# Performance work log

Hardware: AMD Instinct MI355X
Metric: run time of the kernel (lower is better)

Reference implementation:

```python
import jax, jax.numpy as jnp
import numpy as np

N_NODES = 100000
N_EDGES = 640000
NODE_D = 128   # node_emb_dim == edge_type_emb_dim (required by reverse-net input dim)
MSG_D = 128


def setup_inputs() -> dict:
    key = jax.random.key(0)
    ks = jax.random.split(key, 10)
    cat_d = 3 * NODE_D  # 2*node_emb + edge_type_emb
    s_msg = 1.0 / np.sqrt(cat_d)
    s_upd = 1.0 / np.sqrt(MSG_D)
    return {
        "node_features": jax.random.normal(ks[0], (N_NODES, NODE_D), jnp.float32),
        "edge_features": jax.random.normal(ks[1], (N_EDGES, NODE_D), jnp.float32),
        "from_idx": jax.random.randint(ks[2], (N_EDGES,), 0, N_NODES, jnp.int32),
        "to_idx": jax.random.randint(ks[3], (N_EDGES,), 0, N_NODES, jnp.int32),
        # message net (Linear + ReLU)
        "W_msg": jax.random.uniform(ks[4], (cat_d, MSG_D), jnp.float32, -s_msg, s_msg),
        "b_msg": jnp.zeros((MSG_D,), jnp.float32),
        # reverse message net (separate params)
        "W_rev": jax.random.uniform(ks[5], (cat_d, MSG_D), jnp.float32, -s_msg, s_msg),
        "b_rev": jnp.zeros((MSG_D,), jnp.float32),
        # node-update MLP (Linear + ReLU), residual update
        "W_upd": jax.random.uniform(ks[6], (MSG_D, NODE_D), jnp.float32, -s_upd, s_upd),
        "b_upd": jnp.zeros((NODE_D,), jnp.float32),
    }


def reference(node_features, edge_features, from_idx, to_idx,
              W_msg, b_msg, W_rev, b_rev, W_upd, b_upd):
    # gather endpoints and concat with edge features: [n_edges, 3*node_d]
    edge_inputs = jnp.concatenate(
        [node_features[from_idx], node_features[to_idx], edge_features], axis=-1)
    # forward + reverse message nets (same inputs, different params), summed
    messages = (jax.nn.relu(edge_inputs @ W_msg + b_msg)
                + jax.nn.relu(edge_inputs @ W_rev + b_rev))
    # scatter-sum into destination nodes: [n_nodes, msg_d]
    aggregated = jax.ops.segment_sum(messages, to_idx, num_segments=N_NODES)
    # residual node update: node + MLP(agg)
    return node_features + jax.nn.relu(aggregated @ W_upd + b_upd)
```

## Files before the change

kernel.cpp:

```cpp
#include <hip/hip_runtime.h>
#include <hip/hip_bf16.h>

#define N_NODES 100000
#define N_EDGES 640000

typedef __bf16 bf16_t;
typedef __bf16 bf16x8 __attribute__((ext_vector_type(8)));
typedef float f32x4 __attribute__((ext_vector_type(4)));
typedef float f4 __attribute__((ext_vector_type(4)));
typedef unsigned int u32x4 __attribute__((ext_vector_type(4)));

__device__ __forceinline__ float bflo(unsigned int u) { return __uint_as_float(u << 16); }
__device__ __forceinline__ float bfhi(unsigned int u) { return __uint_as_float(u & 0xffff0000u); }
__device__ __forceinline__ unsigned int bfpack(float a, float b) {
    union { bf16_t h[2]; unsigned int u; } pk;
    pk.h[0] = (bf16_t)a; pk.h[1] = (bf16_t)b;
    return pk.u;
}

__global__ void hist_kernel(const int* __restrict__ to_idx, int* __restrict__ hist) {
    int e = blockIdx.x * 256 + threadIdx.x;
    if (e < N_EDGES) atomicAdd(&hist[to_idx[e]], 1);
}

#define SCAN_CH 1000

__global__ __launch_bounds__(1024)
void scan_reduce_kernel(const int* __restrict__ hist, int* __restrict__ bsum) {
    __shared__ int red[1024];
    int b = blockIdx.x, t = threadIdx.x;
    int v = (t < SCAN_CH) ? hist[b * SCAN_CH + t] : 0;
    red[t] = v;
    __syncthreads();
    for (int off = 512; off > 0; off >>= 1) {
        if (t < off) red[t] += red[t + off];
        __syncthreads();
    }
    if (t == 0) bsum[b] = red[0];
}

__global__ __launch_bounds__(128)
void scan_base_kernel(const int* __restrict__ bsum, int* __restrict__ bbase) {
    __shared__ int s[128];
    int t = threadIdx.x;
    int v = (t < 100) ? bsum[t] : 0;
    s[t] = v;
    __syncthreads();
    for (int off = 1; off < 128; off <<= 1) {
        int u = (t >= off) ? s[t - off] : 0;
        __syncthreads();
        s[t] += u;
        __syncthreads();
    }
    if (t < 100) bbase[t] = s[t] - v;
}

__global__ __launch_bounds__(1024)
void scan_final_kernel(const int* __restrict__ hist,
                       const int* __restrict__ bbase,
                       int* __restrict__ cursor,
                       int* __restrict__ row_start) {
    __shared__ int s[1024];
    int b = blockIdx.x, t = threadIdx.x;
    int v = (t < SCAN_CH) ? hist[b * SCAN_CH + t] : 0;
    s[t] = v;
    __syncthreads();
    for (int off = 1; off < 1024; off <<= 1) {
        int u = (t >= off) ? s[t - off] : 0;
        __syncthreads();
        s[t] += u;
        __syncthreads();
    }
    int excl = bbase[b] + s[t] - v;
    if (t < SCAN_CH) {
        cursor[b * SCAN_CH + t] = excl;
        row_start[b * SCAN_CH + t] = excl;
    }
    if (b == 99 && t == SCAN_CH - 1) row_start[N_NODES] = excl + v;
}

__global__ void inv_scatter_kernel(const int* __restrict__ to_idx,
                                   int* __restrict__ cursor,
                                   int* __restrict__ inv) {
    int e = blockIdx.x * 256 + threadIdx.x;
    if (e < N_EDGES) {
        int pos = atomicAdd(&cursor[to_idx[e]], 1);
        inv[e] = pos;
    }
}

__global__ void prep_w_new(const float* __restrict__ Wmsg,
                           const float* __restrict__ Wrev,
                           const float* __restrict__ Wupd,
                           bf16_t* __restrict__ Wt1,
                           bf16_t* __restrict__ WtE,
                           bf16_t* __restrict__ WtU) {
    int idx = blockIdx.x * 256 + threadIdx.x;
    if (idx < 512 * 128) {
        int p = idx >> 7, k = idx & 127;
        int blk = p >> 7, c = p & 127;
        float v;
        if (blk == 0)      v = Wmsg[k * 128 + c];
        else if (blk == 1) v = Wrev[k * 128 + c];
        else if (blk == 2) v = Wmsg[(128 + k) * 128 + c];
        else               v = Wrev[(128 + k) * 128 + c];
        Wt1[idx] = (bf16_t)v;
    }
    if (idx < 256 * 128) {
        int p = idx >> 7, k = idx & 127;
        float v = (p < 128) ? Wmsg[(256 + k) * 128 + p]
                            : Wrev[(256 + k) * 128 + (p - 128)];
        WtE[idx] = (bf16_t)v;
    }
    if (idx < 128 * 128) {
        int n = idx >> 7, p = idx & 127;
        int colp = 32 * (p >> 5) + ((p >> 1) & 15) + 16 * (p & 1);
        WtU[idx] = (bf16_t)Wupd[colp * 128 + n];
    }
}

__global__ __launch_bounds__(512, 4)
void proj_node_kernel(const float* __restrict__ nodef,
                      const bf16_t* __restrict__ Wt1,
                      unsigned int* __restrict__ A_u) {
    __shared__ char lds_raw[64 * 256];
    const int tid = threadIdx.x;
    const int nb = blockIdx.x * 64;
    const int by = blockIdx.y;

#pragma unroll
    for (int j = 0; j < 4; ++j) {
        int linear = tid + 512 * j;
        int r = linear >> 5, q = linear & 31;
        int node = nb + r;
        f4 v = (f4){0.f, 0.f, 0.f, 0.f};
        if (node < N_NODES)
            v = *reinterpret_cast<const f4*>(nodef + (size_t)node * 128 + q * 4);
        union { bf16_t b[4]; uint2 u; } pk;
        pk.b[0] = (bf16_t)v[0]; pk.b[1] = (bf16_t)v[1];
        pk.b[2] = (bf16_t)v[2]; pk.b[3] = (bf16_t)v[3];
        int byte = (r * 256 + q * 8) ^ ((r & 7) << 4);
        *reinterpret_cast<uint2*>(lds_raw + byte) = pk.u;
    }
    __syncthreads();

    const int wv = tid >> 6;
    const int wr = wv >> 2, wc = wv & 3;
    const int lane = tid & 63;
    const int lhi = lane >> 4, llo = lane & 15;

    f32x4 acc[2][4];
#pragma unroll
    for (int m = 0; m < 2; ++m)
#pragma unroll
        for (int n = 0; n < 4; ++n)
            acc[m][n] = (f32x4){0.f, 0.f, 0.f, 0.f};

    const bf16_t* bptr[4];
#pragma unroll
    for (int n = 0; n < 4; ++n) {
        int colb = (n < 2) ? (wc * 32 + 16 * n) : (128 + wc * 32 + 16 * (n - 2));
        bptr[n] = Wt1 + (size_t)(by * 256 + colb + llo) * 128 + lhi * 8;
    }

#pragma unroll
    for (int k0 = 0; k0 < 4; ++k0) {
        bf16x8 a[2], b[4];
#pragma unroll
        for (int m = 0; m < 2; ++m) {
            int ra = wr * 32 + 16 * m + llo;
            int byte = (ra * 256 + (k0 * 32 + lhi * 8) * 2) ^ ((ra & 7) << 4);
            a[m] = *reinterpret_cast<const bf16x8*>(lds_raw + byte);
        }
#pragma unroll
        for (int n = 0; n < 4; ++n)
            b[n] = *reinterpret_cast<const bf16x8*>(bptr[n] + k0 * 32);
#pragma unroll
        for (int m = 0; m < 2; ++m)
#pragma unroll
            for (int n = 0; n < 4; ++n)
                acc[m][n] = __builtin_amdgcn_mfma_f32_16x16x32_bf16(a[m], b[n], acc[m][n], 0, 0, 0);
    }

    const int wli = wc * 16 + llo;
#pragma unroll
    for (int m = 0; m < 2; ++m) {
        int rbase = wr * 32 + 16 * m + lhi * 4;
#pragma unroll
        for (int r = 0; r < 4; ++r) {
            int node = nb + rbase + r;
            if (node < N_NODES) {
                size_t base = (size_t)node * 256 + by * 128;
                uint2 pr;
                pr.x = bfpack(acc[m][0][r], acc[m][1][r]);
                pr.y = bfpack(acc[m][2][r], acc[m][3][r]);
                *reinterpret_cast<uint2*>(A_u + base + 2 * wli) = pr;
            }
        }
    }
}

__global__ __launch_bounds__(256, 4)
void edge_fused_kernel(const float* __restrict__ edgef,
                       const int* __restrict__ from_idx,
                       const int* __restrict__ to_idx,
                       const int* __restrict__ inv,
                       const unsigned int* __restrict__ A_u,
                       const bf16_t* __restrict__ WtE,
                       const float* __restrict__ b_msg,
                       const float* __restrict__ b_rev,
                       unsigned int* __restrict__ msgs_u) {
    __shared__ char lds_raw[2][8192];
    __shared__ int s_from[128], s_dst[128], s_inv[128];

    const int tid = threadIdx.x;
    const size_t eb0 = (size_t)blockIdx.x * 128;

    if (tid < 128) {
        s_from[tid] = from_idx[eb0 + tid];
        s_dst[tid]  = to_idx[eb0 + tid];
        s_inv[tid]  = inv[eb0 + tid];
    }

    const int wc = tid >> 6;
    const int lane = tid & 63;
    const int lhi = lane >> 4, llo = lane & 15;
    const int wli = wc * 16 + llo;

    const bf16_t* bptr[4];
#pragma unroll
    for (int n = 0; n < 4; ++n) {
        int colb = (n < 2) ? (wc * 32 + 16 * n) : (128 + wc * 32 + 16 * (n - 2));
        bptr[n] = WtE + (size_t)(colb + llo) * 128 + lhi * 8;
    }

    const int c0 = wc * 32 + llo;
    const float bm0 = b_msg[c0], bm1 = b_msg[c0 + 16];
    const float br0 = b_rev[c0], br1 = b_rev[c0 + 16];

    f4 st[4];
#pragma unroll
    for (int j = 0; j < 4; ++j) {
        int lin = tid + 256 * j, r = lin >> 5, q = lin & 31;
        st[j] = *reinterpret_cast<const f4*>(edgef + (eb0 + r) * 128 + q * 4);
    }
#pragma unroll
    for (int j = 0; j < 4; ++j) {
        int lin = tid + 256 * j, r = lin >> 5, q = lin & 31;
        union { bf16_t b[4]; uint2 u; } pk;
        pk.b[0] = (bf16_t)st[j][0]; pk.b[1] = (bf16_t)st[j][1];
        pk.b[2] = (bf16_t)st[j][2]; pk.b[3] = (bf16_t)st[j][3];
        int byte = (r * 256 + q * 8) ^ ((r & 7) << 4);
        *reinterpret_cast<uint2*>(&lds_raw[0][0] + byte) = pk.u;
    }
    __syncthreads();

#pragma unroll
    for (int t = 0; t < 4; ++t) {
        const int cur = t & 1;

        bf16x8 bA[2][4];
#pragma unroll
        for (int k0 = 0; k0 < 2; ++k0)
#pragma unroll
            for (int n = 0; n < 4; ++n)
                bA[k0][n] = *reinterpret_cast<const bf16x8*>(bptr[n] + k0 * 32);

        uint2 gF[2][4], gT[2][4];
#pragma unroll
        for (int m = 0; m < 2; ++m)
#pragma unroll
            for (int r = 0; r < 4; ++r) {
                int rr = t * 32 + 16 * m + lhi * 4 + r;
                gF[m][r] = *reinterpret_cast<const uint2*>(
                    A_u + (size_t)s_from[rr] * 256 + 2 * wli);
                gT[m][r] = *reinterpret_cast<const uint2*>(
                    A_u + (size_t)s_dst[rr] * 256 + 128 + 2 * wli);
            }

        if (t < 3) {
#pragma unroll
            for (int j = 0; j < 4; ++j) {
                int lin = tid + 256 * j, r = lin >> 5, q = lin & 31;
                st[j] = *reinterpret_cast<const f4*>(
                    edgef + (eb0 + (size_t)(t + 1) * 32 + r) * 128 + q * 4);
            }
        }

        f32x4 acc[2][4];
#pragma unroll
        for (int m = 0; m < 2; ++m)
#pragma unroll
            for (int n = 0; n < 4; ++n)
                acc[m][n] = (f32x4){0.f, 0.f, 0.f, 0.f};
#pragma unroll
        for (int k0 = 0; k0 < 2; ++k0) {
            bf16x8 a[2];
#pragma unroll
            for (int m = 0; m < 2; ++m) {
                int ra = 16 * m + llo;
                int byte = (ra * 256 + (k0 * 32 + lhi * 8) * 2) ^ ((ra & 7) << 4);
                a[m] = *reinterpret_cast<const bf16x8*>(&lds_raw[cur][0] + byte);
            }
#pragma unroll
            for (int m = 0; m < 2; ++m)
#pragma unroll
                for (int n = 0; n < 4; ++n)
                    acc[m][n] = __builtin_amdgcn_mfma_f32_16x16x32_bf16(a[m], bA[k0][n], acc[m][n], 0, 0, 0);
        }

#pragma unroll
        for (int k0 = 0; k0 < 2; ++k0)
#pragma unroll
            for (int n = 0; n < 4; ++n)
                bA[k0][n] = *reinterpret_cast<const bf16x8*>(bptr[n] + (2 + k0) * 32);

#pragma unroll
        for (int k0 = 0; k0 < 2; ++k0) {
            bf16x8 a[2];
#pragma unroll
            for (int m = 0; m < 2; ++m) {
                int ra = 16 * m + llo;
                int byte = (ra * 256 + ((2 + k0) * 32 + lhi * 8) * 2) ^ ((ra & 7) << 4);
                a[m] = *reinterpret_cast<const bf16x8*>(&lds_raw[cur][0] + byte);
            }
#pragma unroll
            for (int m = 0; m < 2; ++m)
#pragma unroll
                for (int n = 0; n < 4; ++n)
                    acc[m][n] = __builtin_amdgcn_mfma_f32_16x16x32_bf16(a[m], bA[k0][n], acc[m][n], 0, 0, 0);
        }

        if (t < 3) {
#pragma unroll
            for (int j = 0; j < 4; ++j) {
                int lin = tid + 256 * j, r = lin >> 5, q = lin & 31;
                union { bf16_t b[4]; uint2 u; } pk;
                pk.b[0] = (bf16_t)st[j][0]; pk.b[1] = (bf16_t)st[j][1];
                pk.b[2] = (bf16_t)st[j][2]; pk.b[3] = (bf16_t)st[j][3];
                int byte = (r * 256 + q * 8) ^ ((r & 7) << 4);
                *reinterpret_cast<uint2*>(&lds_raw[cur ^ 1][0] + byte) = pk.u;
            }
        }

#pragma unroll
        for (int m = 0; m < 2; ++m)
#pragma unroll
            for (int r = 0; r < 4; ++r) {
                int rr = t * 32 + 16 * m + lhi * 4 + r;
                float m0 = fmaxf(acc[m][0][r] + bm0 + bflo(gF[m][r].x) + bflo(gT[m][r].x), 0.f);
                float m1 = fmaxf(acc[m][1][r] + bm1 + bfhi(gF[m][r].x) + bfhi(gT[m][r].x), 0.f);
                float r0 = fmaxf(acc[m][2][r] + br0 + bflo(gF[m][r].y) + bflo(gT[m][r].y), 0.f);
                float r1 = fmaxf(acc[m][3][r] + br1 + bfhi(gF[m][r].y) + bfhi(gT[m][r].y), 0.f);
                msgs_u[(size_t)s_inv[rr] * 64 + wli] = bfpack(m0 + r0, m1 + r1);
            }

        __syncthreads();
    }
}

__global__ __launch_bounds__(256, 4)
void node_upd_kernel(const unsigned int* __restrict__ msgs_u,
                     const int* __restrict__ row_start,
                     const float* __restrict__ nodef,
                     const bf16_t* __restrict__ WtU,
                     const float* __restrict__ b_upd,
                     float* __restrict__ out) {
    __shared__ char lds_raw[64 * 256];
    __shared__ int s_rs[65];

    const int tid = threadIdx.x;
    const int nb = blockIdx.x * 64;

    if (tid < 65) {
        int nid = nb + tid;
        s_rs[tid] = (nid <= N_NODES) ? row_start[nid] : N_EDGES;
    }
    __syncthreads();

    {
        const int r = tid >> 2;
        const int q = tid & 3;
        float s[32];
#pragma unroll
        for (int i = 0; i < 32; ++i) s[i] = 0.f;
        const int rs = s_rs[r], re = s_rs[r + 1];
        int e = rs;
        for (; e + 1 < re; e += 2) {
            const u32x4* p0 = reinterpret_cast<const u32x4*>(msgs_u + (size_t)e * 64 + q * 16);
            const u32x4* p1 = reinterpret_cast<const u32x4*>(msgs_u + (size_t)(e + 1) * 64 + q * 16);
            u32x4 w0[4], w1[4];
#pragma unroll
            for (int i = 0; i < 4; ++i) { w0[i] = p0[i]; w1[i] = p1[i]; }
#pragma unroll
            for (int i = 0; i < 4; ++i) {
                s[8*i+0] += bflo(w0[i][0]) + bflo(w1[i][0]);
                s[8*i+1] += bfhi(w0[i][0]) + bfhi(w1[i][0]);
                s[8*i+2] += bflo(w0[i][1]) + bflo(w1[i][1]);
                s[8*i+3] += bfhi(w0[i][1]) + bfhi(w1[i][1]);
                s[8*i+4] += bflo(w0[i][2]) + bflo(w1[i][2]);
                s[8*i+5] += bfhi(w0[i][2]) + bfhi(w1[i][2]);
                s[8*i+6] += bflo(w0[i][3]) + bflo(w1[i][3]);
                s[8*i+7] += bfhi(w0[i][3]) + bfhi(w1[i][3]);
            }
        }
        if (e < re) {
            const u32x4* p = reinterpret_cast<const u32x4*>(msgs_u + (size_t)e * 64 + q * 16);
#pragma unroll
            for (int i = 0; i < 4; ++i) {
                u32x4 w = p[i];
                s[8*i+0] += bflo(w[0]); s[8*i+1] += bfhi(w[0]);
                s[8*i+2] += bflo(w[1]); s[8*i+3] += bfhi(w[1]);
                s[8*i+4] += bflo(w[2]); s[8*i+5] += bfhi(w[2]);
                s[8*i+6] += bflo(w[3]); s[8*i+7] += bfhi(w[3]);
            }
        }
#pragma unroll
        for (int i = 0; i < 4; ++i) {
            union { bf16_t b[8]; u32x4 u; } pk;
#pragma unroll
            for (int w = 0; w < 8; ++w) pk.b[w] = (bf16_t)s[8*i + w];
            int byte = (r * 256 + q * 64 + i * 16) ^ ((r & 7) << 4);
            *reinterpret_cast<u32x4*>(lds_raw + byte) = pk.u;
        }
    }
    __syncthreads();

    const int wv = tid >> 6;
    const int lane = tid & 63;
    const int lhi = lane >> 4, llo = lane & 15;

    f32x4 acc[4][2];
#pragma unroll
    for (int m = 0; m < 4; ++m)
#pragma unroll
        for (int n = 0; n < 2; ++n)
            acc[m][n] = (f32x4){0.f, 0.f, 0.f, 0.f};

#pragma unroll
    for (int k0 = 0; k0 < 4; ++k0) {
        bf16x8 a[4], b[2];
#pragma unroll
        for (int m = 0; m < 4; ++m) {
            int ra = 16 * m + llo;
            int byte = (ra * 256 + (k0 * 32 + lhi * 8) * 2) ^ ((ra & 7) << 4);
            a[m] = *reinterpret_cast<const bf16x8*>(lds_raw + byte);
        }
#pragma unroll
        for (int n = 0; n < 2; ++n) {
            int col = wv * 32 + 16 * n + llo;
            b[n] = *reinterpret_cast<const bf16x8*>(WtU + (size_t)col * 128 + k0 * 32 + lhi * 8);
        }
#pragma unroll
        for (int m = 0; m < 4; ++m)
#pragma unroll
            for (int n = 0; n < 2; ++n)
                acc[m][n] = __builtin_amdgcn_mfma_f32_16x16x32_bf16(a[m], b[n], acc[m][n], 0, 0, 0);
    }

#pragma unroll
    for (int m = 0; m < 4; ++m) {
        int rbase = 16 * m + lhi * 4;
#pragma unroll
        for (int r = 0; r < 4; ++r) {
            int i = nb + rbase + r;
            if (i < N_NODES) {
#pragma unroll
                for (int n = 0; n < 2; ++n) {
                    int c = wv * 32 + 16 * n + llo;
                    out[(size_t)i * 128 + c] =
                        nodef[(size_t)i * 128 + c]
                        + fmaxf(acc[m][n][r] + b_upd[c], 0.f);
                }
            }
        }
    }
}

extern "C" void kernel_launch(void* const* d_in, const int* in_sizes, int n_in,
                              void* d_out, int out_size, void* d_ws, size_t ws_size,
                              hipStream_t stream) {
    const float* nodef    = (const float*)d_in[0];
    const float* edgef    = (const float*)d_in[1];
    const int*   from_idx = (const int*)d_in[2];
    const int*   to_idx   = (const int*)d_in[3];
    const float* Wmsg     = (const float*)d_in[4];
    const float* bmsg     = (const float*)d_in[5];
    const float* Wrev     = (const float*)d_in[6];
    const float* brev     = (const float*)d_in[7];
    const float* Wupd     = (const float*)d_in[8];
    const float* bupd     = (const float*)d_in[9];
    float* out = (float*)d_out;
    char* ws = (char*)d_ws;

    unsigned int* A_u      = (unsigned int*)ws;
    unsigned int* msgs_u   = (unsigned int*)(ws + 102400000);
    bf16_t*       Wt1      = (bf16_t*)(ws + 266240000);
    bf16_t*       WtE      = (bf16_t*)(ws + 266371072);
    bf16_t*       WtU      = (bf16_t*)(ws + 266436608);
    int*          hist     = (int*)(ws + 266469376);
    int*          cursor   = (int*)(ws + 266869376);
    int*          rowstart = (int*)(ws + 267269376);
    int*          inv      = (int*)(ws + 267669392);
    int*          bsum     = (int*)(ws + 270229392);
    int*          bbase    = (int*)(ws + 270229792);

    hipMemsetAsync(hist, 0, (size_t)N_NODES * sizeof(int), stream);
    prep_w_new<<<256, 256, 0, stream>>>(Wmsg, Wrev, Wupd, Wt1, WtE, WtU);
    hist_kernel<<<(N_EDGES + 255) / 256, 256, 0, stream>>>(to_idx, hist);
    scan_reduce_kernel<<<100, 1024, 0, stream>>>(hist, bsum);
    scan_base_kernel<<<1, 128, 0, stream>>>(bsum, bbase);
    scan_final_kernel<<<100, 1024, 0, stream>>>(hist, bbase, cursor, rowstart);
    inv_scatter_kernel<<<(N_EDGES + 255) / 256, 256, 0, stream>>>(to_idx, cursor, inv);
    proj_node_kernel<<<dim3((N_NODES + 63) / 64, 2), 512, 0, stream>>>(nodef, Wt1, A_u);
    edge_fused_kernel<<<N_EDGES / 128, 256, 0, stream>>>(
        edgef, from_idx, to_idx, inv, A_u, WtE, bmsg, brev, msgs_u);
    node_upd_kernel<<<(N_NODES + 63) / 64, 256, 0, stream>>>(
        msgs_u, rowstart, nodef, WtU, bupd, out);
}
```

Before: 457.5 us.

## Simplify edge kernel to one 32-edge tile per block without software pipelining

Measured after the change: 446.1 us. 2.5% less time.

```diff
diff --git a/kernel.cpp b/kernel.cpp
--- a/kernel.cpp
+++ b/kernel.cpp
@@ -210,23 +210,56 @@
                        const float* __restrict__ b_msg,
                        const float* __restrict__ b_rev,
                        unsigned int* __restrict__ msgs_u) {
-    __shared__ char lds_raw[2][8192];
-    __shared__ int s_from[128], s_dst[128], s_inv[128];
+    __shared__ char lds_raw[32 * 256];
+    __shared__ int s_from[32], s_dst[32], s_inv[32];
 
     const int tid = threadIdx.x;
-    const size_t eb0 = (size_t)blockIdx.x * 128;
-
-    if (tid < 128) {
-        s_from[tid] = from_idx[eb0 + tid];
-        s_dst[tid]  = to_idx[eb0 + tid];
-        s_inv[tid]  = inv[eb0 + tid];
-    }
+    const int eb = blockIdx.x * 32;
+
+    if (tid < 32) {
+        s_from[tid] = from_idx[eb + tid];
+        s_dst[tid]  = to_idx[eb + tid];
+        s_inv[tid]  = inv[eb + tid];
+    }
+
+#pragma unroll
+    for (int j = 0; j < 4; ++j) {
+        int linear = tid + 256 * j;
+        int r = linear >> 5, q = linear & 31;
+        f4 v = __builtin_nontemporal_load(
+            reinterpret_cast<const f4*>(edgef + (size_t)(eb + r) * 128 + q * 4));
+        union { bf16_t b[4]; uint2 u; } pk;
+        pk.b[0] = (bf16_t)v[0]; pk.b[1] = (bf16_t)v[1];
+        pk.b[2] = (bf16_t)v[2]; pk.b[3] = (bf16_t)v[3];
+        int byte = (r * 256 + q * 8) ^ ((r & 7) << 4);
+        *reinterpret_cast<uint2*>(lds_raw + byte) = pk.u;
+    }
+    __syncthreads();
 
     const int wc = tid >> 6;
     const int lane = tid & 63;
     const int lhi = lane >> 4, llo = lane & 15;
     const int wli = wc * 16 + llo;
 
+    uint2 gF[2][4], gT[2][4];
+#pragma unroll
+    for (int m = 0; m < 2; ++m)
+#pragma unroll
+        for (int r = 0; r < 4; ++r) {
+            int rr = 16 * m + lhi * 4 + r;
+            gF[m][r] = *reinterpret_cast<const uint2*>(
+                A_u + (size_t)s_from[rr] * 256 + 2 * wli);
+            gT[m][r] = *reinterpret_cast<const uint2*>(
+                A_u + (size_t)s_dst[rr] * 256 + 128 + 2 * wli);
+        }
+
+    f32x4 acc[2][4];
+#pragma unroll
+    for (int m = 0; m < 2; ++m)
+#pragma unroll
+        for (int n = 0; n < 4; ++n)
+            acc[m][n] = (f32x4){0.f, 0.f, 0.f, 0.f};
+
     const bf16_t* bptr[4];
 #pragma unroll
     for (int n = 0; n < 4; ++n) {
@@ -234,128 +267,39 @@
         bptr[n] = WtE + (size_t)(colb + llo) * 128 + lhi * 8;
     }
 
+#pragma unroll
+    for (int k0 = 0; k0 < 4; ++k0) {
+        bf16x8 a[2], b[4];
+#pragma unroll
+        for (int m = 0; m < 2; ++m) {
+            int ra = 16 * m + llo;
+            int byte = (ra * 256 + (k0 * 32 + lhi * 8) * 2) ^ ((ra & 7) << 4);
+            a[m] = *reinterpret_cast<const bf16x8*>(lds_raw + byte);
+        }
+#pragma unroll
+        for (int n = 0; n < 4; ++n)
+            b[n] = *reinterpret_cast<const bf16x8*>(bptr[n] + k0 * 32);
+#pragma unroll
+        for (int m = 0; m < 2; ++m)
+#pragma unroll
+            for (int n = 0; n < 4; ++n)
+                acc[m][n] = __builtin_amdgcn_mfma_f32_16x16x32_bf16(a[m], b[n], acc[m][n], 0, 0, 0);
+    }
+
     const int c0 = wc * 32 + llo;
     const float bm0 = b_msg[c0], bm1 = b_msg[c0 + 16];
     const float br0 = b_rev[c0], br1 = b_rev[c0 + 16];
-
-    f4 st[4];
-#pragma unroll
-    for (int j = 0; j < 4; ++j) {
-        int lin = tid + 256 * j, r = lin >> 5, q = lin & 31;
-        st[j] = *reinterpret_cast<const f4*>(edgef + (eb0 + r) * 128 + q * 4);
-    }
-#pragma unroll
-    for (int j = 0; j < 4; ++j) {
-        int lin = tid + 256 * j, r = lin >> 5, q = lin & 31;
-        union { bf16_t b[4]; uint2 u; } pk;
-        pk.b[0] = (bf16_t)st[j][0]; pk.b[1] = (bf16_t)st[j][1];
-        pk.b[2] = (bf16_t)st[j][2]; pk.b[3] = (bf16_t)st[j][3];
-        int byte = (r * 256 + q * 8) ^ ((r & 7) << 4);
-        *reinterpret_cast<uint2*>(&lds_raw[0][0] + byte) = pk.u;
-    }
-    __syncthreads();
-
-#pragma unroll
-    for (int t = 0; t < 4; ++t) {
-        const int cur = t & 1;
-
-        bf16x8 bA[2][4];
-#pragma unroll
-        for (int k0 = 0; k0 < 2; ++k0)
-#pragma unroll
-            for (int n = 0; n < 4; ++n)
-                bA[k0][n] = *reinterpret_cast<const bf16x8*>(bptr[n] + k0 * 32);
-
-        uint2 gF[2][4], gT[2][4];
-#pragma unroll
-        for (int m = 0; m < 2; ++m)
-#pragma unroll
-            for (int r = 0; r < 4; ++r) {
-                int rr = t * 32 + 16 * m + lhi * 4 + r;
-                gF[m][r] = *reinterpret_cast<const uint2*>(
-                    A_u + (size_t)s_from[rr] * 256 + 2 * wli);
-                gT[m][r] = *reinterpret_cast<const uint2*>(
-                    A_u + (size_t)s_dst[rr] * 256 + 128 + 2 * wli);
-            }
-
-        if (t < 3) {
-#pragma unroll
-            for (int j = 0; j < 4; ++j) {
-                int lin = tid + 256 * j, r = lin >> 5, q = lin & 31;
-                st[j] = *reinterpret_cast<const f4*>(
-                    edgef + (eb0 + (size_t)(t + 1) * 32 + r) * 128 + q * 4);
-            }
-        }
-
-        f32x4 acc[2][4];
-#pragma unroll
-        for (int m = 0; m < 2; ++m)
-#pragma unroll
-            for (int n = 0; n < 4; ++n)
-                acc[m][n] = (f32x4){0.f, 0.f, 0.f, 0.f};
-#pragma unroll
-        for (int k0 = 0; k0 < 2; ++k0) {
-            bf16x8 a[2];
-#pragma unroll
-            for (int m = 0; m < 2; ++m) {
-                int ra = 16 * m + llo;
-                int byte = (ra * 256 + (k0 * 32 + lhi * 8) * 2) ^ ((ra & 7) << 4);
-                a[m] = *reinterpret_cast<const bf16x8*>(&lds_raw[cur][0] + byte);
-            }
-#pragma unroll
-            for (int m = 0; m < 2; ++m)
-#pragma unroll
-                for (int n = 0; n < 4; ++n)
-                    acc[m][n] = __builtin_amdgcn_mfma_f32_16x16x32_bf16(a[m], bA[k0][n], acc[m][n], 0, 0, 0);
-        }
-
-#pragma unroll
-        for (int k0 = 0; k0 < 2; ++k0)
-#pragma unroll
-            for (int n = 0; n < 4; ++n)
-                bA[k0][n] = *reinterpret_cast<const bf16x8*>(bptr[n] + (2 + k0) * 32);
-
-#pragma unroll
-        for (int k0 = 0; k0 < 2; ++k0) {
-            bf16x8 a[2];
-#pragma unroll
-            for (int m = 0; m < 2; ++m) {
-                int ra = 16 * m + llo;
-                int byte = (ra * 256 + ((2 + k0) * 32 + lhi * 8) * 2) ^ ((ra & 7) << 4);
-                a[m] = *reinterpret_cast<const bf16x8*>(&lds_raw[cur][0] + byte);
-            }
-#pragma unroll
-            for (int m = 0; m < 2; ++m)
-#pragma unroll
-                for (int n = 0; n < 4; ++n)
-                    acc[m][n] = __builtin_amdgcn_mfma_f32_16x16x32_bf16(a[m], bA[k0][n], acc[m][n], 0, 0, 0);
-        }
-
-        if (t < 3) {
-#pragma unroll
-            for (int j = 0; j < 4; ++j) {
-                int lin = tid + 256 * j, r = lin >> 5, q = lin & 31;
-                union { bf16_t b[4]; uint2 u; } pk;
-                pk.b[0] = (bf16_t)st[j][0]; pk.b[1] = (bf16_t)st[j][1];
-                pk.b[2] = (bf16_t)st[j][2]; pk.b[3] = (bf16_t)st[j][3];
-                int byte = (r * 256 + q * 8) ^ ((r & 7) << 4);
-                *reinterpret_cast<uint2*>(&lds_raw[cur ^ 1][0] + byte) = pk.u;
-            }
-        }
-
-#pragma unroll
-        for (int m = 0; m < 2; ++m)
-#pragma unroll
-            for (int r = 0; r < 4; ++r) {
-                int rr = t * 32 + 16 * m + lhi * 4 + r;
-                float m0 = fmaxf(acc[m][0][r] + bm0 + bflo(gF[m][r].x) + bflo(gT[m][r].x), 0.f);
-                float m1 = fmaxf(acc[m][1][r] + bm1 + bfhi(gF[m][r].x) + bfhi(gT[m][r].x), 0.f);
-                float r0 = fmaxf(acc[m][2][r] + br0 + bflo(gF[m][r].y) + bflo(gT[m][r].y), 0.f);
-                float r1 = fmaxf(acc[m][3][r] + br1 + bfhi(gF[m][r].y) + bfhi(gT[m][r].y), 0.f);
-                msgs_u[(size_t)s_inv[rr] * 64 + wli] = bfpack(m0 + r0, m1 + r1);
-            }
-
-        __syncthreads();
+#pragma unroll
+    for (int m = 0; m < 2; ++m) {
+#pragma unroll
+        for (int r = 0; r < 4; ++r) {
+            int rr = 16 * m + lhi * 4 + r;
+            float m0 = fmaxf(acc[m][0][r] + bm0 + bflo(gF[m][r].x) + bflo(gT[m][r].x), 0.f);
+            float m1 = fmaxf(acc[m][1][r] + bm1 + bfhi(gF[m][r].x) + bfhi(gT[m][r].x), 0.f);
+            float r0 = fmaxf(acc[m][2][r] + br0 + bflo(gF[m][r].y) + bflo(gT[m][r].y), 0.f);
+            float r1 = fmaxf(acc[m][3][r] + br1 + bfhi(gF[m][r].y) + bfhi(gT[m][r].y), 0.f);
+            msgs_u[(size_t)s_inv[rr] * 64 + wli] = bfpack(m0 + r0, m1 + r1);
+        }
     }
 }
 
@@ -385,26 +329,7 @@
 #pragma unroll
         for (int i = 0; i < 32; ++i) s[i] = 0.f;
         const int rs = s_rs[r], re = s_rs[r + 1];
-        int e = rs;
-        for (; e + 1 < re; e += 2) {
-            const u32x4* p0 = reinterpret_cast<const u32x4*>(msgs_u + (size_t)e * 64 + q * 16);
-            const u32x4* p1 = reinterpret_cast<const u32x4*>(msgs_u + (size_t)(e + 1) * 64 + q * 16);
-            u32x4 w0[4], w1[4];
-#pragma unroll
-            for (int i = 0; i < 4; ++i) { w0[i] = p0[i]; w1[i] = p1[i]; }
-#pragma unroll
-            for (int i = 0; i < 4; ++i) {
-                s[8*i+0] += bflo(w0[i][0]) + bflo(w1[i][0]);
-                s[8*i+1] += bfhi(w0[i][0]) + bfhi(w1[i][0]);
-                s[8*i+2] += bflo(w0[i][1]) + bflo(w1[i][1]);
-                s[8*i+3] += bfhi(w0[i][1]) + bfhi(w1[i][1]);
-                s[8*i+4] += bflo(w0[i][2]) + bflo(w1[i][2]);
-                s[8*i+5] += bfhi(w0[i][2]) + bfhi(w1[i][2]);
-                s[8*i+6] += bflo(w0[i][3]) + bflo(w1[i][3]);
-                s[8*i+7] += bfhi(w0[i][3]) + bfhi(w1[i][3]);
-            }
-        }
-        if (e < re) {
+        for (int e = rs; e < re; ++e) {
             const u32x4* p = reinterpret_cast<const u32x4*>(msgs_u + (size_t)e * 64 + q * 16);
 #pragma unroll
             for (int i = 0; i < 4; ++i) {
@@ -513,7 +438,7 @@
     scan_final_kernel<<<100, 1024, 0, stream>>>(hist, bbase, cursor, rowstart);
     inv_scatter_kernel<<<(N_EDGES + 255) / 256, 256, 0, stream>>>(to_idx, cursor, inv);
     proj_node_kernel<<<dim3((N_NODES + 63) / 64, 2), 512, 0, stream>>>(nodef, Wt1, A_u);
-    edge_fused_kernel<<<N_EDGES / 128, 256, 0, stream>>>(
+    edge_fused_kernel<<<N_EDGES / 32, 256, 0, stream>>>(
         edgef, from_idx, to_idx, inv, A_u, WtE, bmsg, brev, msgs_u);
     node_upd_kernel<<<(N_NODES + 63) / 64, 256, 0, stream>>>(
         msgs_u, rowstart, nodef, WtU, bupd, out);
```
